# Optimization experiments

Measured on AMD Instinct MI355X. Metric: run time of the kernel, lower is better.

The kernel has to match this reference:

```python
import jax, jax.numpy as jnp
import numpy as np

N, E, D_IN, HID, HEADS, TS_OUT = 100000, 200000, 165, 64, 8, 5
HD1 = HID // HEADS  # 8 per-head channels in layer 1
HD2 = HID           # 64 per-head channels in layer 2 (concat=False -> mean)


def _glorot(key, shape):
    fan_in, fan_out = shape[0], shape[1]
    s = np.sqrt(6.0 / (fan_in + fan_out)).astype(np.float32)
    return jax.random.uniform(key, shape, jnp.float32, -s, s)


def setup_inputs() -> dict:
    key = jax.random.key(0)
    ks = jax.random.split(key, 24)
    inp = {
        "x": jax.random.normal(ks[0], (N, D_IN), jnp.float32),
        "edge_index": jax.random.randint(ks[1], (2, E), 0, N, jnp.int32),
        "timestamp_target": jax.random.randint(ks[2], (N,), 0, TS_OUT, jnp.int32),
        "node_target": jax.random.randint(ks[3], (N,), 0, 2, jnp.int32),
        "node_mask": jax.random.randint(ks[4], (N,), 0, 2, jnp.int32).astype(jnp.bool_),
        # GATConv layer 1: in=165 -> 8 heads x 8 ch, concat -> 64
        "W1": _glorot(ks[5], (D_IN, HEADS * HD1)),
        "att_src1": _glorot(ks[6], (HEADS, HD1)),
        "att_dst1": _glorot(ks[7], (HEADS, HD1)),
        "b1": jnp.zeros((HEADS * HD1,), jnp.float32),
        # GATConv layer 2: in=64 -> 8 heads x 64 ch, mean -> 64
        "W2": _glorot(ks[8], (HID, HEADS * HD2)),
        "att_src2": _glorot(ks[9], (HEADS, HD2)),
        "att_dst2": _glorot(ks[10], (HEADS, HD2)),
        "b2": jnp.zeros((HD2,), jnp.float32),
        # timestamp predictor MLP
        "ts_w1": _glorot(ks[11], (HID, HID)), "ts_b1": jnp.zeros((HID,), jnp.float32),
        "ts_w2": _glorot(ks[12], (HID, TS_OUT)), "ts_b2": jnp.zeros((TS_OUT,), jnp.float32),
        # class predictor MLP
        "cls_w1": _glorot(ks[13], (HID, HID)), "cls_b1": jnp.zeros((HID,), jnp.float32),
        "cls_w2": _glorot(ks[14], (HID, 2)), "cls_b2": jnp.zeros((2,), jnp.float32),
    }
    return inp


def _gat_layer(x, src, dst, n, W, a_src, a_dst, b, concat):
    H, C = a_src.shape
    h = (x @ W).reshape(n, H, C)                      # [N,H,C]
    a_s = (h * a_src).sum(-1)                         # [N,H]
    a_d = (h * a_dst).sum(-1)                         # [N,H]
    alpha = jax.nn.leaky_relu(a_s[src] + a_d[dst], 0.2)   # [E,H]
    amax = jax.ops.segment_max(alpha, dst, num_segments=n)
    ea = jnp.exp(alpha - amax[dst])
    denom = jax.ops.segment_sum(ea, dst, num_segments=n)
    a = ea / (denom[dst] + 1e-16)                     # segment softmax over incoming edges
    out = jax.ops.segment_sum(h[src] * a[:, :, None], dst, num_segments=n)  # [N,H,C]
    out = out.reshape(n, H * C) if concat else out.mean(axis=1)
    return out + b


def _ce(logits, targets):
    lp = jax.nn.log_softmax(logits, axis=-1)
    return -jnp.take_along_axis(lp, targets[:, None].astype(jnp.int32), axis=1)[:, 0]


def reference(x, edge_index, timestamp_target, node_target, node_mask,
              W1, att_src1, att_dst1, b1, W2, att_src2, att_dst2, b2,
              ts_w1, ts_b1, ts_w2, ts_b2, cls_w1, cls_b1, cls_w2, cls_b2):
    n = x.shape[0]
    loops = jnp.arange(n, dtype=edge_index.dtype)
    src = jnp.concatenate([edge_index[0], loops])     # add self loops (PyG default)
    dst = jnp.concatenate([edge_index[1], loops])
    h = _gat_layer(x, src, dst, n, W1, att_src1, att_dst1, b1, True)   # [N,64]
    h = _gat_layer(h, src, dst, n, W2, att_src2, att_dst2, b2, False)  # [N,64]
    # gradient reversal is identity in the forward pass
    ts_pred = jax.nn.relu(h @ ts_w1 + ts_b1) @ ts_w2 + ts_b2           # [N,5]
    cls_pred = jax.nn.relu(h @ cls_w1 + cls_b1) @ cls_w2 + cls_b2      # [N,2]
    ts_loss = _ce(ts_pred, timestamp_target).mean()
    m = node_mask.astype(jnp.float32)
    cls_loss = (_ce(cls_pred, node_target) * m).sum() / m.sum()
    return cls_loss + 1.0 * ts_loss
```

## Files before the change

### kernel.cpp

```cpp
#include <hip/hip_runtime.h>
#include <hip/hip_bf16.h>

#define NN 100000
#define NE 200000
#define NT (NE + NN)
#define DIN 165
#define PREPB 128
#define INITB 391
#define PACKB 32
#define W1PB 24
#define MISCGRID (PREPB + INITB + PACKB + W1PB)
#define NODEB 1563
#define XDW ((size_t)NN * DIN)
#define G1ROWS 32
#define G1NDMA 21
#define L2ROWS 32

typedef __attribute__((ext_vector_type(8))) short bf16x8_t;
typedef __attribute__((ext_vector_type(4))) float f32x4_t;
typedef _Float16 h2_t __attribute__((ext_vector_type(2)));
typedef _Float16 f16x8_t __attribute__((ext_vector_type(8)));

#define AS1 __attribute__((address_space(1)))
#define AS3 __attribute__((address_space(3)))

static __device__ __forceinline__ unsigned short f2bf(float f) {
    __hip_bfloat16 b = __float2bfloat16(f);
    return *(unsigned short*)&b;
}
static __device__ __forceinline__ float bfu(unsigned short u) {
    __hip_bfloat16 b = *(__hip_bfloat16*)&u;
    return __bfloat162float(b);
}
static __device__ __forceinline__ unsigned pkh2(float a, float b) {
    h2_t v; v[0] = (_Float16)a; v[1] = (_Float16)b;
    return *(unsigned*)&v;
}


__global__ __launch_bounds__(256) void k_misc(const float* W2, const float* a2s, const float* a2d,
                                              float* wsd, __hip_bfloat16* W2pT,
                                              int* cnt, int* fill,
                                              const float* tsw1, const float* cw1,
                                              __hip_bfloat16* wB,
                                              const float* W1, unsigned* W1pT, float* zbuf) {
    int b = blockIdx.x;
    int tid = threadIdx.x;
    if (b < PREPB) {
        int i = b * 256 + tid;
        int c = i >> 9, j = i & 511;
        int hh = j >> 6, kk = j & 63;
        W2pT[i] = __float2bfloat16(W2[kk * 512 + hh * 64 + c]);
        if (b == 0) zbuf[tid] = 0.f;
        if (i < 512) {
            int h = i >> 6, k = i & 63;
            float s = 0.f, d = 0.f;
            for (int cc = 0; cc < 64; cc++) {
                float w = W2[k * 512 + h * 64 + cc];
                s += w * a2s[h * 64 + cc];
                d += w * a2d[h * 64 + cc];
            }
            wsd[i] = s; wsd[512 + i] = d;
        }
    } else if (b < PREPB + INITB) {
        int i = (b - PREPB) * 256 + tid;
        if (i < NN) { cnt[i] = 0; fill[i] = 0; }
    } else if (b < PREPB + INITB + PACKB) {
        int i = (b - PREPB - INITB) * 256 + tid;
        if (i < 8192) {
            int c = i >> 6, k = i & 63;
            float v = (c < 64) ? tsw1[k * 64 + c] : cw1[k * 64 + (c - 64)];
            wB[i] = __float2bfloat16(v);
        }
    } else {
        int i = (b - PREPB - INITB - PACKB) * 256 + tid;
        if (i < 6144) {
            int c = i / 96, kp = i - c * 96;
            int k = 2 * kp;
            float f0 = (k < DIN) ? W1[k * 64 + c] : 0.f;
            float f1 = (k + 1 < DIN) ? W1[(k + 1) * 64 + c] : 0.f;
            W1pT[i] = pkh2(f0, f1);
        }
    }
}


__global__ __launch_bounds__(256) void k_count(const int* dstE, int* cnt) {
    int e = blockIdx.x * 256 + threadIdx.x;
    if (e < NE) atomicAdd(&cnt[dstE[e]], 1);
}

__global__ __launch_bounds__(256) void k_scanA(const int* cnt, int* rowptr, int* bsum) {
    __shared__ int sm[256];
    int t = threadIdx.x;
    int base = blockIdx.x * 1024;
    int v[4]; int s = 0;
    for (int i = 0; i < 4; i++) {
        int idx = base + t * 4 + i;
        v[i] = (idx < NN) ? (cnt[idx] + 1) : 0;
        s += v[i];
    }
    sm[t] = s; __syncthreads();
    for (int off = 1; off < 256; off <<= 1) {
        int x = (t >= off) ? sm[t - off] : 0;
        __syncthreads();
        sm[t] += x;
        __syncthreads();
    }
    int run = sm[t] - s;
    for (int i = 0; i < 4; i++) {
        run += v[i];
        int idx = base + t * 4 + i;
        if (idx < NN) rowptr[idx + 1] = run;
    }
    if (t == 255) bsum[blockIdx.x] = sm[255];
}

__global__ __launch_bounds__(64) void k_scanB(int* bsum, int nb) {
    int lane = threadIdx.x;
    int v0 = (lane < nb) ? bsum[lane] : 0;
    int v1 = (64 + lane < nb) ? bsum[64 + lane] : 0;
    int s0 = v0;
    for (int off = 1; off < 64; off <<= 1) { int t = __shfl_up(s0, off); if (lane >= off) s0 += t; }
    int tot0 = __shfl(s0, 63);
    int s1 = v1;
    for (int off = 1; off < 64; off <<= 1) { int t = __shfl_up(s1, off); if (lane >= off) s1 += t; }
    if (lane < nb) bsum[lane] = s0 - v0;
    if (64 + lane < nb) bsum[64 + lane] = tot0 + s1 - v1;
}

__global__ __launch_bounds__(256) void k_scanC(const int* bsum, int* rowptr) {
    int i = blockIdx.x * 256 + threadIdx.x;
    if (i < NN) rowptr[i + 1] += bsum[i >> 10];
    if (i == 0) rowptr[0] = 0;
}

__global__ __launch_bounds__(256) void k_fill(const int* srcE, const int* dstE,
                                              const int* rowptr, int* fill, int* col, int* rowv) {
    int i = blockIdx.x * 256 + threadIdx.x;
    if (i >= NT) return;
    int s, d;
    if (i < NE) { s = srcE[i]; d = dstE[i]; }
    else        { s = i - NE; d = s; }
    int p = rowptr[d] + atomicAdd(&fill[d], 1);
    col[p] = s;
    rowv[p] = d;
}


__global__ __launch_bounds__(128) void k_gemm1(const float* x, const unsigned* W1pT,
                                               const float* att_s, const float* att_d,
                                               const float* zsrc,
                                               __hip_bfloat16* h1b, float* aad1) {
    __shared__ float X[G1NDMA * 256];
    int tid = threadIdx.x;
    int l = tid & 63, w = tid >> 6;
    int n0 = blockIdx.x * G1ROWS;
    int frow = l & 15, kg = l >> 4;

    size_t tb = (size_t)n0 * DIN;
    for (int i = w; i < G1NDMA; i += 2) {
        size_t gd = tb + (size_t)i * 256 + (size_t)l * 4;
        const float* g = (gd + 4 <= XDW) ? (x + gd) : (zsrc + l * 4);
        __builtin_amdgcn_global_load_lds((const AS1 float*)g,
                                         (AS3 float*)(X + i * 256), 16, 0, 0);
    }
    uint4 B[6][4];
    #pragma unroll
    for (int s = 0; s < 6; s++)
        #pragma unroll
        for (int t = 0; t < 4; t++)
            B[s][t] = *(const uint4*)&W1pT[(t * 16 + frow) * 96 + s * 16 + kg * 4];
    __syncthreads();

    f32x4_t acc[4] = {};
    int rbase = (w * 16 + frow) * DIN + kg * 8;
    #pragma unroll
    for (int s = 0; s < 6; s++) {
        f16x8_t av;
        #pragma unroll
        for (int j = 0; j < 8; j++) av[j] = (_Float16)X[rbase + s * 32 + j];
        #pragma unroll
        for (int t = 0; t < 4; t++)
            acc[t] = __builtin_amdgcn_mfma_f32_16x16x32_f16(av, *(f16x8_t*)&B[s][t], acc[t], 0, 0, 0);
    }

    int nw = n0 + w * 16;
    float asv[4], adv[4];
    #pragma unroll
    for (int t = 0; t < 4; t++) {
        int c = t * 16 + frow;
        asv[t] = att_s[c]; adv[t] = att_d[c];
    }
    int hb = (l >> 3) & 1;
    #pragma unroll
    for (int q = 0; q < 4; q++) {
        int n = nw + kg * 4 + q;
        #pragma unroll
        for (int t = 0; t < 4; t++) {
            float sv = acc[t][q] * asv[t];
            float dv = acc[t][q] * adv[t];
            sv += __shfl_xor(sv, 1); sv += __shfl_xor(sv, 2); sv += __shfl_xor(sv, 4);
            dv += __shfl_xor(dv, 1); dv += __shfl_xor(dv, 2); dv += __shfl_xor(dv, 4);
            if ((l & 7) == 0) {
                int h = t * 2 + hb;
                aad1[(size_t)n * 16 + h]     = sv;
                aad1[(size_t)n * 16 + 8 + h] = dv;
            }
        }
    }

    __syncthreads();
    unsigned short* Hw = (unsigned short*)X + w * 1152;
    #pragma unroll
    for (int t = 0; t < 4; t++)
        #pragma unroll
        for (int q = 0; q < 4; q++)
            Hw[(kg * 4 + q) * 72 + t * 16 + frow] = f2bf(acc[t][q]);
    int rr = l >> 2, cc = l & 3;
    int n2 = nw + rr;
    unsigned short* dst = (unsigned short*)h1b + (size_t)n2 * 64 + cc * 16;
    *(uint4*)dst       = *(const uint4*)&Hw[rr * 72 + cc * 16];
    *(uint4*)(dst + 8) = *(const uint4*)&Hw[rr * 72 + cc * 16 + 8];
}


__global__ __launch_bounds__(256) void k_edgew(const float* aad, const int* col, const int* rowv,
                                               __hip_bfloat16* web) {
    int e = blockIdx.x * 256 + threadIdx.x;
    if (e >= NT) return;
    int s = col[e], d = rowv[e];
    float4 s0 = *(const float4*)&aad[(size_t)s * 16];
    float4 s1 = *(const float4*)&aad[(size_t)s * 16 + 4];
    float4 dd0 = *(const float4*)&aad[(size_t)d * 16 + 8];
    float4 dd1 = *(const float4*)&aad[(size_t)d * 16 + 12];
    float as[8] = {s0.x, s0.y, s0.z, s0.w, s1.x, s1.y, s1.z, s1.w};
    float ad[8] = {dd0.x, dd0.y, dd0.z, dd0.w, dd1.x, dd1.y, dd1.z, dd1.w};
    unsigned p[4];
    #pragma unroll
    for (int q = 0; q < 4; q++) {
        float a0 = as[2*q]   + ad[2*q];
        float a1 = as[2*q+1] + ad[2*q+1];
        a0 = a0 > 0.f ? a0 : 0.2f * a0;
        a1 = a1 > 0.f ? a1 : 0.2f * a1;
        p[q] = (unsigned)f2bf(__expf(a0)) | ((unsigned)f2bf(__expf(a1)) << 16);
    }
    *(uint4*)&web[(size_t)e * 8] = make_uint4(p[0], p[1], p[2], p[3]);
}


__global__ __launch_bounds__(256) void k_agg1(const __hip_bfloat16* h1b, const __hip_bfloat16* we1b,
                                              const int* rowptr, const int* col,
                                              const float* b1, __hip_bfloat16* out1b) {
    int tid = threadIdx.x;
    int q = tid & 15;
    int n = blockIdx.x * 16 + (tid >> 4);
    int hq = q >> 1;
    const unsigned short* h1u = (const unsigned short*)h1b;
    const unsigned short* weu = (const unsigned short*)we1b;
    int rs = rowptr[n], re = rowptr[n + 1];
    float acc0 = 0.f, acc1 = 0.f, acc2 = 0.f, acc3 = 0.f, den = 0.f;
    for (int eb = rs; eb < re; eb += 4) {
        int c4[4];
        #pragma unroll
        for (int j = 0; j < 4; j++) c4[j] = col[min(eb + j, re - 1)];
        #pragma unroll
        for (int j = 0; j < 4; j++) {
            int e = min(eb + j, re - 1);
            float wv = bfu(weu[(size_t)e * 8 + hq]);
            wv = (eb + j < re) ? wv : 0.f;
            uint2 hv = *(const uint2*)&h1u[(size_t)c4[j] * 64 + q * 4];
            den  += wv;
            acc0 += wv * bfu((unsigned short)(hv.x & 0xffff));
            acc1 += wv * bfu((unsigned short)(hv.x >> 16));
            acc2 += wv * bfu((unsigned short)(hv.y & 0xffff));
            acc3 += wv * bfu((unsigned short)(hv.y >> 16));
        }
    }
    float4 bb = *(const float4*)&b1[q * 4];
    float dd = den + 1e-16f;
    unsigned short* ou = (unsigned short*)out1b;
    unsigned p0 = (unsigned)f2bf(acc0 / dd + bb.x) | ((unsigned)f2bf(acc1 / dd + bb.y) << 16);
    unsigned p1 = (unsigned)f2bf(acc2 / dd + bb.z) | ((unsigned)f2bf(acc3 / dd + bb.w) << 16);
    *(uint2*)&ou[(size_t)n * 64 + q * 4] = make_uint2(p0, p1);
}


__global__ __launch_bounds__(256) void k_att2(const __hip_bfloat16* out1b, const float* wsd,
                                              float* aad2) {
    __shared__ float t[64][65];
    int tid = threadIdx.x;
    int n0 = blockIdx.x * 64;
    const unsigned short* o1u = (const unsigned short*)out1b;
    #pragma unroll
    for (int l = 0; l < 4; l++) {
        int q = tid + l * 256;
        int r = q >> 4, c4 = q & 15;
        int n = n0 + r;
        uint2 v = make_uint2(0, 0);
        if (n < NN) v = *(const uint2*)&o1u[(size_t)n * 64 + c4 * 4];
        t[r][c4 * 4 + 0] = bfu((unsigned short)(v.x & 0xffff));
        t[r][c4 * 4 + 1] = bfu((unsigned short)(v.x >> 16));
        t[r][c4 * 4 + 2] = bfu((unsigned short)(v.y & 0xffff));
        t[r][c4 * 4 + 3] = bfu((unsigned short)(v.y >> 16));
    }
    __syncthreads();
    int lane = tid & 63;
    int j0 = __builtin_amdgcn_readfirstlane((tid >> 6) * 4);
    int n = n0 + lane;
    float a0 = 0.f, a1 = 0.f, a2 = 0.f, a3 = 0.f;
    #pragma unroll 8
    for (int k = 0; k < 64; k++) {
        float ov = t[lane][k];
        a0 += ov * wsd[(j0 + 0) * 64 + k];
        a1 += ov * wsd[(j0 + 1) * 64 + k];
        a2 += ov * wsd[(j0 + 2) * 64 + k];
        a3 += ov * wsd[(j0 + 3) * 64 + k];
    }
    if (n < NN) *(float4*)&aad2[(size_t)n * 16 + j0] = make_float4(a0, a1, a2, a3);
}


__global__ __launch_bounds__(256) void k_l2f(const __hip_bfloat16* out1b, const __hip_bfloat16* we2b,
                                             const int* rowptr, const int* col,
                                             const __hip_bfloat16* W2pT, const float* b2,
                                             const __hip_bfloat16* wB,
                                             const float* tsb1, const float* cb1,
                                             const float* tsw2, const float* tsb2,
                                             const float* cw2, const float* cb2,
                                             const int* tst, const int* ctg, const unsigned char* msk,
                                             float* part) {
    __shared__ unsigned short Ax[L2ROWS * 512];
    __shared__ float red[4][3];
    int tid = threadIdx.x;
    int l = tid & 63, w = tid >> 6;
    int n0 = blockIdx.x * L2ROWS;
    int frow = l & 15, kg = l >> 4;

    const unsigned short* o1u = (const unsigned short*)out1b;
    const unsigned short* weu = (const unsigned short*)we2b;
    int q4 = tid & 15;
    #pragma unroll 1
    for (int pass = 0; pass < 2; pass++) {
        int j = pass * 16 + (tid >> 4);
        int n = n0 + j;
        int rs = rowptr[n], re = rowptr[n + 1];
        float acc[8][4];
        float den[8];
        #pragma unroll
        for (int h = 0; h < 8; h++) {
            den[h] = 0.f;
            #pragma unroll
            for (int c = 0; c < 4; c++) acc[h][c] = 0.f;
        }
        for (int eb = rs; eb < re; eb += 4) {
            int c4[4];
            #pragma unroll
            for (int jj = 0; jj < 4; jj++) c4[jj] = col[min(eb + jj, re - 1)];
            #pragma unroll
            for (int jj = 0; jj < 4; jj++) {
                int e = min(eb + jj, re - 1);
                uint4 wv = *(const uint4*)&weu[(size_t)e * 8];
                uint2 hv = *(const uint2*)&o1u[(size_t)c4[jj] * 64 + q4 * 4];
                float vm = (eb + jj < re) ? 1.f : 0.f;
                float hc0 = bfu((unsigned short)(hv.x & 0xffff));
                float hc1 = bfu((unsigned short)(hv.x >> 16));
                float hc2 = bfu((unsigned short)(hv.y & 0xffff));
                float hc3 = bfu((unsigned short)(hv.y >> 16));
                float wt[8] = {bfu((unsigned short)(wv.x & 0xffff)), bfu((unsigned short)(wv.x >> 16)),
                               bfu((unsigned short)(wv.y & 0xffff)), bfu((unsigned short)(wv.y >> 16)),
                               bfu((unsigned short)(wv.z & 0xffff)), bfu((unsigned short)(wv.z >> 16)),
                               bfu((unsigned short)(wv.w & 0xffff)), bfu((unsigned short)(wv.w >> 16))};
                #pragma unroll
                for (int h = 0; h < 8; h++) {
                    float ww = wt[h] * vm;
                    den[h] += ww;
                    acc[h][0] += ww * hc0;
                    acc[h][1] += ww * hc1;
                    acc[h][2] += ww * hc2;
                    acc[h][3] += ww * hc3;
                }
            }
        }
        #pragma unroll
        for (int h = 0; h < 8; h++) {
            float dd = den[h] + 1e-16f;
            unsigned lo = (unsigned)f2bf(acc[h][0] / dd) | ((unsigned)f2bf(acc[h][1] / dd) << 16);
            unsigned hi = (unsigned)f2bf(acc[h][2] / dd) | ((unsigned)f2bf(acc[h][3] / dd) << 16);
            int blk = (h * 8 + (q4 >> 1)) ^ (j & 7);
            *(uint2*)&Ax[j * 512 + blk * 8 + (q4 & 1) * 4] = make_uint2(lo, hi);
        }
    }
    __syncthreads();

    const unsigned short* Bg = (const unsigned short*)W2pT;
    int r0 = (w & 1) * 16;
    int c0 = (w >> 1) * 32;
    f32x4_t gacc[2] = {};
    uint4 rBa00, rBa01, rBa10, rBa11;
    rBa00 = *(const uint4*)&Bg[(size_t)(c0 + frow) * 512 + 0 * 32 + kg * 8];
    rBa01 = *(const uint4*)&Bg[(size_t)(c0 + frow) * 512 + 1 * 32 + kg * 8];
    rBa10 = *(const uint4*)&Bg[(size_t)(c0 + 16 + frow) * 512 + 0 * 32 + kg * 8];
    rBa11 = *(const uint4*)&Bg[(size_t)(c0 + 16 + frow) * 512 + 1 * 32 + kg * 8];
    #pragma unroll
    for (int k0 = 0; k0 < 512; k0 += 64) {
        uint4 rBb00, rBb01, rBb10, rBb11;
        if (k0 < 448) {
            int kn = k0 + 64;
            rBb00 = *(const uint4*)&Bg[(size_t)(c0 + frow) * 512 + kn + 0 * 32 + kg * 8];
            rBb01 = *(const uint4*)&Bg[(size_t)(c0 + frow) * 512 + kn + 1 * 32 + kg * 8];
            rBb10 = *(const uint4*)&Bg[(size_t)(c0 + 16 + frow) * 512 + kn + 0 * 32 + kg * 8];
            rBb11 = *(const uint4*)&Bg[(size_t)(c0 + 16 + frow) * 512 + kn + 1 * 32 + kg * 8];
        }
        #pragma unroll
        for (int kk = 0; kk < 2; kk++) {
            int bidx = (k0 >> 3) + kk * 4 + kg;
            int blk = bidx ^ (frow & 7);
            bf16x8_t a = *(const bf16x8_t*)&Ax[(r0 + frow) * 512 + blk * 8];
            gacc[0] = __builtin_amdgcn_mfma_f32_16x16x32_bf16(
                a, *(bf16x8_t*)(kk == 0 ? &rBa00 : &rBa01), gacc[0], 0, 0, 0);
            gacc[1] = __builtin_amdgcn_mfma_f32_16x16x32_bf16(
                a, *(bf16x8_t*)(kk == 0 ? &rBa10 : &rBa11), gacc[1], 0, 0, 0);
        }
        rBa00 = rBb00; rBa01 = rBb01; rBa10 = rBb10; rBa11 = rBb11;
    }
    __syncthreads();

    unsigned short* o2L = Ax;
    #pragma unroll
    for (int t = 0; t < 2; t++) {
        float bias = b2[c0 + t * 16 + frow];
        f32x4_t g = gacc[t];
        #pragma unroll
        for (int q = 0; q < 4; q++)
            o2L[(r0 + kg * 4 + q) * 72 + c0 + t * 16 + frow] = f2bf(0.125f * g[q] + bias);
    }
    __syncthreads();
    const unsigned short* wBu = (const unsigned short*)wB;
    int m0 = (w & 1) * 16;
    int h0 = (w >> 1) * 64;
    f32x4_t a2c[4] = {};
    #pragma unroll
    for (int kk = 0; kk < 2; kk++) {
        bf16x8_t a2 = *(const bf16x8_t*)&o2L[(m0 + frow) * 72 + kk * 32 + kg * 8];
        #pragma unroll
        for (int t2 = 0; t2 < 4; t2++) {
            bf16x8_t bf = *(const bf16x8_t*)&wBu[(h0 + t2 * 16 + frow) * 64 + kk * 32 + kg * 8];
            a2c[t2] = __builtin_amdgcn_mfma_f32_16x16x32_bf16(a2, bf, a2c[t2], 0, 0, 0);
        }
    }

    float tsl = 0.f, cll = 0.f, mval = 0.f;
    if ((w >> 1) == 0) {
        float lg[4][5];
        #pragma unroll
        for (int q = 0; q < 4; q++)
            #pragma unroll
            for (int t = 0; t < 5; t++) lg[q][t] = 0.f;
        #pragma unroll
        for (int t2 = 0; t2 < 4; t2++) {
            int c = t2 * 16 + frow;
            float bb = tsb1[c];
            float w0 = tsw2[c * 5 + 0], w1 = tsw2[c * 5 + 1], w2 = tsw2[c * 5 + 2],
                  w3 = tsw2[c * 5 + 3], w4 = tsw2[c * 5 + 4];
            #pragma unroll
            for (int q = 0; q < 4; q++) {
                float v = fmaxf(a2c[t2][q] + bb, 0.f);
                lg[q][0] += v * w0; lg[q][1] += v * w1; lg[q][2] += v * w2;
                lg[q][3] += v * w3; lg[q][4] += v * w4;
            }
        }
        #pragma unroll
        for (int q = 0; q < 4; q++)
            #pragma unroll
            for (int t = 0; t < 5; t++) {
                lg[q][t] += __shfl_xor(lg[q][t], 1);
                lg[q][t] += __shfl_xor(lg[q][t], 2);
                lg[q][t] += __shfl_xor(lg[q][t], 4);
                lg[q][t] += __shfl_xor(lg[q][t], 8);
            }
        if (frow == 0) {
            #pragma unroll
            for (int q = 0; q < 4; q++) {
                int n = n0 + m0 + kg * 4 + q;
                float L[5];
                #pragma unroll
                for (int t = 0; t < 5; t++) L[t] = lg[q][t] + tsb2[t];
                float mx = fmaxf(fmaxf(fmaxf(L[0], L[1]), fmaxf(L[2], L[3])), L[4]);
                float se = 0.f;
                #pragma unroll
                for (int t = 0; t < 5; t++) se += __expf(L[t] - mx);
                int tg = tst[n];
                float pick = 0.f;
                #pragma unroll
                for (int t = 0; t < 5; t++) pick += (t == tg) ? L[t] : 0.f;
                tsl += mx + __logf(se) - pick;
            }
        }
    } else {
        float lc[4][2];
        #pragma unroll
        for (int q = 0; q < 4; q++) { lc[q][0] = 0.f; lc[q][1] = 0.f; }
        #pragma unroll
        for (int t2 = 0; t2 < 4; t2++) {
            int c = t2 * 16 + frow;
            float bb = cb1[c];
            float u0 = cw2[c * 2], u1 = cw2[c * 2 + 1];
            #pragma unroll
            for (int q = 0; q < 4; q++) {
                float v = fmaxf(a2c[t2][q] + bb, 0.f);
                lc[q][0] += v * u0; lc[q][1] += v * u1;
            }
        }
        #pragma unroll
        for (int q = 0; q < 4; q++)
            #pragma unroll
            for (int t = 0; t < 2; t++) {
                lc[q][t] += __shfl_xor(lc[q][t], 1);
                lc[q][t] += __shfl_xor(lc[q][t], 2);
                lc[q][t] += __shfl_xor(lc[q][t], 4);
                lc[q][t] += __shfl_xor(lc[q][t], 8);
            }
        if (frow == 0) {
            #pragma unroll
            for (int q = 0; q < 4; q++) {
                int n = n0 + m0 + kg * 4 + q;
                float C0 = lc[q][0] + cb2[0];
                float C1 = lc[q][1] + cb2[1];
                float mx2 = fmaxf(C0, C1);
                float lse2 = mx2 + __logf(__expf(C0 - mx2) + __expf(C1 - mx2));
                float mv = msk[n] ? 1.f : 0.f;
                float pick2 = ctg[n] ? C1 : C0;
                cll += (lse2 - pick2) * mv;
                mval += mv;
            }
        }
    }
    #pragma unroll
    for (int off = 1; off < 64; off <<= 1) {
        tsl  += __shfl_xor(tsl, off);
        cll  += __shfl_xor(cll, off);
        mval += __shfl_xor(mval, off);
    }
    if (l == 0) { red[w][0] = tsl; red[w][1] = cll; red[w][2] = mval; }
    __syncthreads();
    if (tid == 0) {
        part[blockIdx.x * 3 + 0] = red[0][0] + red[1][0] + red[2][0] + red[3][0];
        part[blockIdx.x * 3 + 1] = red[0][1] + red[1][1] + red[2][1] + red[3][1];
        part[blockIdx.x * 3 + 2] = red[0][2] + red[1][2] + red[2][2] + red[3][2];
    }
}

__global__ __launch_bounds__(256) void k_final(const float* part, float* out, int nb) {
    __shared__ float sm[3][256];
    int tid = threadIdx.x;
    float a = 0, b = 0, c = 0;
    for (int i = tid; i < nb; i += 256) { a += part[i*3]; b += part[i*3+1]; c += part[i*3+2]; }
    sm[0][tid] = a; sm[1][tid] = b; sm[2][tid] = c;
    __syncthreads();
    for (int s = 128; s > 0; s >>= 1) {
        if (tid < s) {
            sm[0][tid] += sm[0][tid + s];
            sm[1][tid] += sm[1][tid + s];
            sm[2][tid] += sm[2][tid + s];
        }
        __syncthreads();
    }
    if (tid == 0) out[0] = sm[1][0] / sm[2][0] + sm[0][0] / (float)NN;
}


extern "C" void kernel_launch(void* const* d_in, const int* in_sizes, int n_in,
                              void* d_out, int out_size, void* d_ws, size_t ws_size,
                              hipStream_t stream) {
    const float* x    = (const float*)d_in[0];
    const int*   ei   = (const int*)d_in[1];
    const int*   tst  = (const int*)d_in[2];
    const int*   ctg  = (const int*)d_in[3];
    const unsigned char* msk = (const unsigned char*)d_in[4];
    const float* W1   = (const float*)d_in[5];
    const float* a1s  = (const float*)d_in[6];
    const float* a1d  = (const float*)d_in[7];
    const float* b1   = (const float*)d_in[8];
    const float* W2   = (const float*)d_in[9];
    const float* a2s  = (const float*)d_in[10];
    const float* a2d  = (const float*)d_in[11];
    const float* b2   = (const float*)d_in[12];
    const float* tsw1 = (const float*)d_in[13];
    const float* tsb1 = (const float*)d_in[14];
    const float* tsw2 = (const float*)d_in[15];
    const float* tsb2 = (const float*)d_in[16];
    const float* cw1  = (const float*)d_in[17];
    const float* cb1  = (const float*)d_in[18];
    const float* cw2  = (const float*)d_in[19];
    const float* cb2  = (const float*)d_in[20];
    const int* srcE = ei;
    const int* dstE = ei + NE;

    char* ws = (char*)d_ws;
    size_t off = 0;
    auto alloc = [&](size_t b) { size_t o = off; off = (off + b + 255) & ~(size_t)255; return o; };
    int*   cnt    = (int*)(ws + alloc((size_t)NN * 4));
    int*   fill   = (int*)(ws + alloc((size_t)NN * 4));
    int*   rowptr = (int*)(ws + alloc((size_t)(NN + 1) * 4));
    int*   bsum   = (int*)(ws + alloc(128 * 4));
    int*   col    = (int*)(ws + alloc((size_t)NT * 4));
    int*   rowv   = (int*)(ws + alloc((size_t)NT * 4));
    float* aad1   = (float*)(ws + alloc((size_t)NN * 16 * 4));
    __hip_bfloat16* out1b = (__hip_bfloat16*)(ws + alloc((size_t)NN * 64 * 2));
    float* aad2   = (float*)(ws + alloc((size_t)NN * 16 * 4));
    float* wsd    = (float*)(ws + alloc(1024 * 4));
    __hip_bfloat16* W2pT  = (__hip_bfloat16*)(ws + alloc(32768 * 2));
    __hip_bfloat16* wB    = (__hip_bfloat16*)(ws + alloc(8192 * 2));
    unsigned* W1pT = (unsigned*)(ws + alloc(6144 * 4));
    float* zbuf   = (float*)(ws + alloc(256 * 4));
    __hip_bfloat16* h1b   = (__hip_bfloat16*)(ws + alloc((size_t)NN * 64 * 2));
    __hip_bfloat16* web   = (__hip_bfloat16*)(ws + alloc((size_t)NT * 8 * 2));
    float* part   = (float*)(ws + alloc((size_t)(NN / L2ROWS) * 3 * 4));
    (void)ws_size; (void)in_sizes; (void)n_in; (void)out_size;

    int nb_scan = (NN + 1023) / 1024;

    k_misc<<<MISCGRID, 256, 0, stream>>>(W2, a2s, a2d, wsd, W2pT, cnt, fill,
                                         tsw1, cw1, wB, W1, W1pT, zbuf);
    k_count<<<(NE + 255) / 256, 256, 0, stream>>>(dstE, cnt);
    k_scanA<<<nb_scan, 256, 0, stream>>>(cnt, rowptr, bsum);
    k_scanB<<<1, 64, 0, stream>>>(bsum, nb_scan);
    k_scanC<<<(NN + 255) / 256, 256, 0, stream>>>(bsum, rowptr);
    k_fill<<<(NT + 255) / 256, 256, 0, stream>>>(srcE, dstE, rowptr, fill, col, rowv);

    k_gemm1<<<NN / G1ROWS, 128, 0, stream>>>(x, W1pT, a1s, a1d, zbuf, h1b, aad1);
    k_edgew<<<(NT + 255) / 256, 256, 0, stream>>>(aad1, col, rowv, web);
    k_agg1<<<NN / 16, 256, 0, stream>>>(h1b, web, rowptr, col, b1, out1b);
    k_att2<<<NODEB, 256, 0, stream>>>(out1b, wsd, aad2);
    k_edgew<<<(NT + 255) / 256, 256, 0, stream>>>(aad2, col, rowv, web);

    k_l2f<<<NN / L2ROWS, 256, 0, stream>>>(out1b, web, rowptr, col, W2pT, b2, wB,
                                           tsb1, cb1, tsw2, tsb2, cw2, cb2, tst, ctg, msk, part);

    k_final<<<1, 256, 0, stream>>>(part, (float*)d_out, NN / L2ROWS);
}
```

Measured before the change: 199.7 us.

## Fuse att2 into agg1 and split layer-2 aggregation from GEMM in chunks

Computes the layer-2 attention projections inside the layer-1 aggregation kernel with a 16-lane shuffle reduction, which removes the separate att2 kernel and one reread of out1b. The fused layer-2 kernel is split in two. A gather-aggregate kernel writes swizzled bf16 rows to a workspace buffer, and a GEMM+MLP+loss kernel loads those rows into LDS with global_load_lds. This is done in two node chunks to bound the buffer size. The split lets each phase run at its own occupancy, at the cost of extra global traffic (about 50 MB written and read per chunk) and more kernel launches.

```diff
diff --git a/kernel.cpp b/kernel.cpp
--- a/kernel.cpp
+++ b/kernel.cpp
@@ -10,11 +10,11 @@
 #define PACKB 32
 #define W1PB 24
 #define MISCGRID (PREPB + INITB + PACKB + W1PB)
-#define NODEB 1563
 #define XDW ((size_t)NN * DIN)
 #define G1ROWS 32
 #define G1NDMA 21
-#define L2ROWS 32
+#define CHUNKA 49984
+#define GPARTS 3125
 
 typedef __attribute__((ext_vector_type(8))) short bf16x8_t;
 typedef __attribute__((ext_vector_type(4))) float f32x4_t;
@@ -249,9 +249,10 @@
 }
 
 
-__global__ __launch_bounds__(256) void k_agg1(const __hip_bfloat16* h1b, const __hip_bfloat16* we1b,
-                                              const int* rowptr, const int* col,
-                                              const float* b1, __hip_bfloat16* out1b) {
+__global__ __launch_bounds__(256) void k_agg1f(const __hip_bfloat16* h1b, const __hip_bfloat16* we1b,
+                                               const int* rowptr, const int* col,
+                                               const float* b1, const float* wsd,
+                                               __hip_bfloat16* out1b, float* aad2) {
     int tid = threadIdx.x;
     int q = tid & 15;
     int n = blockIdx.x * 16 + (tid >> 4);
@@ -279,117 +280,107 @@
     }
     float4 bb = *(const float4*)&b1[q * 4];
     float dd = den + 1e-16f;
+    unsigned short u0 = f2bf(acc0 / dd + bb.x);
+    unsigned short u1 = f2bf(acc1 / dd + bb.y);
+    unsigned short u2 = f2bf(acc2 / dd + bb.z);
+    unsigned short u3 = f2bf(acc3 / dd + bb.w);
     unsigned short* ou = (unsigned short*)out1b;
-    unsigned p0 = (unsigned)f2bf(acc0 / dd + bb.x) | ((unsigned)f2bf(acc1 / dd + bb.y) << 16);
-    unsigned p1 = (unsigned)f2bf(acc2 / dd + bb.z) | ((unsigned)f2bf(acc3 / dd + bb.w) << 16);
-    *(uint2*)&ou[(size_t)n * 64 + q * 4] = make_uint2(p0, p1);
-}
-
-
-__global__ __launch_bounds__(256) void k_att2(const __hip_bfloat16* out1b, const float* wsd,
-                                              float* aad2) {
-    __shared__ float t[64][65];
+    *(uint2*)&ou[(size_t)n * 64 + q * 4] =
+        make_uint2((unsigned)u0 | ((unsigned)u1 << 16), (unsigned)u2 | ((unsigned)u3 << 16));
+
+    float r0 = bfu(u0), r1 = bfu(u1), r2 = bfu(u2), r3 = bfu(u3);
+    float p[16];
+    #pragma unroll
+    for (int j = 0; j < 16; j++) {
+        float4 wv = *(const float4*)&wsd[j * 64 + q * 4];
+        p[j] = r0 * wv.x + r1 * wv.y + r2 * wv.z + r3 * wv.w;
+    }
+    #pragma unroll
+    for (int s = 1; s < 16; s <<= 1)
+        #pragma unroll
+        for (int j = 0; j < 16; j++) p[j] += __shfl_xor(p[j], s);
+    float myp = 0.f;
+    #pragma unroll
+    for (int j = 0; j < 16; j++) myp = (q == j) ? p[j] : myp;
+    aad2[(size_t)n * 16 + q] = myp;
+}
+
+
+__global__ __launch_bounds__(256) void k_agg2f(const __hip_bfloat16* out1b, const __hip_bfloat16* we2b,
+                                               const int* rowptr, const int* col,
+                                               __hip_bfloat16* aggb, int n0c) {
     int tid = threadIdx.x;
-    int n0 = blockIdx.x * 64;
+    int q4 = tid & 15;
+    int nl = blockIdx.x * 16 + (tid >> 4);
+    int n = n0c + nl;
     const unsigned short* o1u = (const unsigned short*)out1b;
-    #pragma unroll
-    for (int l = 0; l < 4; l++) {
-        int q = tid + l * 256;
-        int r = q >> 4, c4 = q & 15;
-        int n = n0 + r;
-        uint2 v = make_uint2(0, 0);
-        if (n < NN) v = *(const uint2*)&o1u[(size_t)n * 64 + c4 * 4];
-        t[r][c4 * 4 + 0] = bfu((unsigned short)(v.x & 0xffff));
-        t[r][c4 * 4 + 1] = bfu((unsigned short)(v.x >> 16));
-        t[r][c4 * 4 + 2] = bfu((unsigned short)(v.y & 0xffff));
-        t[r][c4 * 4 + 3] = bfu((unsigned short)(v.y >> 16));
-    }
-    __syncthreads();
-    int lane = tid & 63;
-    int j0 = __builtin_amdgcn_readfirstlane((tid >> 6) * 4);
-    int n = n0 + lane;
-    float a0 = 0.f, a1 = 0.f, a2 = 0.f, a3 = 0.f;
-    #pragma unroll 8
-    for (int k = 0; k < 64; k++) {
-        float ov = t[lane][k];
-        a0 += ov * wsd[(j0 + 0) * 64 + k];
-        a1 += ov * wsd[(j0 + 1) * 64 + k];
-        a2 += ov * wsd[(j0 + 2) * 64 + k];
-        a3 += ov * wsd[(j0 + 3) * 64 + k];
-    }
-    if (n < NN) *(float4*)&aad2[(size_t)n * 16 + j0] = make_float4(a0, a1, a2, a3);
-}
-
-
-__global__ __launch_bounds__(256) void k_l2f(const __hip_bfloat16* out1b, const __hip_bfloat16* we2b,
-                                             const int* rowptr, const int* col,
+    const unsigned short* weu = (const unsigned short*)we2b;
+    int rs = rowptr[n], re = rowptr[n + 1];
+    float den[8] = {};
+    float acc[8][4] = {};
+    for (int eb = rs; eb < re; eb += 4) {
+        int c4[4];
+        #pragma unroll
+        for (int jj = 0; jj < 4; jj++) c4[jj] = col[min(eb + jj, re - 1)];
+        #pragma unroll
+        for (int jj = 0; jj < 4; jj++) {
+            int e = min(eb + jj, re - 1);
+            uint4 wv = *(const uint4*)&weu[(size_t)e * 8];
+            uint2 hv = *(const uint2*)&o1u[(size_t)c4[jj] * 64 + q4 * 4];
+            float vm = (eb + jj < re) ? 1.f : 0.f;
+            float hc0 = bfu((unsigned short)(hv.x & 0xffff));
+            float hc1 = bfu((unsigned short)(hv.x >> 16));
+            float hc2 = bfu((unsigned short)(hv.y & 0xffff));
+            float hc3 = bfu((unsigned short)(hv.y >> 16));
+            float wt[8] = {bfu((unsigned short)(wv.x & 0xffff)), bfu((unsigned short)(wv.x >> 16)),
+                           bfu((unsigned short)(wv.y & 0xffff)), bfu((unsigned short)(wv.y >> 16)),
+                           bfu((unsigned short)(wv.z & 0xffff)), bfu((unsigned short)(wv.z >> 16)),
+                           bfu((unsigned short)(wv.w & 0xffff)), bfu((unsigned short)(wv.w >> 16))};
+            #pragma unroll
+            for (int h = 0; h < 8; h++) {
+                float ww = wt[h] * vm;
+                den[h] += ww;
+                acc[h][0] += ww * hc0;
+                acc[h][1] += ww * hc1;
+                acc[h][2] += ww * hc2;
+                acc[h][3] += ww * hc3;
+            }
+        }
+    }
+    unsigned short* au = (unsigned short*)aggb;
+    size_t base = (size_t)nl * 512;
+    #pragma unroll
+    for (int h = 0; h < 8; h++) {
+        float ddv = den[h] + 1e-16f;
+        unsigned lo = (unsigned)f2bf(acc[h][0] / ddv) | ((unsigned)f2bf(acc[h][1] / ddv) << 16);
+        unsigned hi = (unsigned)f2bf(acc[h][2] / ddv) | ((unsigned)f2bf(acc[h][3] / ddv) << 16);
+        int blk = (h * 8 + (q4 >> 1)) ^ (nl & 7);
+        *(uint2*)&au[base + blk * 8 + (q4 & 1) * 4] = make_uint2(lo, hi);
+    }
+}
+
+
+__global__ __launch_bounds__(256) void k_g2m(const __hip_bfloat16* aggb,
                                              const __hip_bfloat16* W2pT, const float* b2,
                                              const __hip_bfloat16* wB,
                                              const float* tsb1, const float* cb1,
                                              const float* tsw2, const float* tsb2,
                                              const float* cw2, const float* cb2,
                                              const int* tst, const int* ctg, const unsigned char* msk,
-                                             float* part) {
-    __shared__ unsigned short Ax[L2ROWS * 512];
+                                             float* part, int n0c, int pbase) {
+    __shared__ unsigned short Ax[32 * 512];
     __shared__ float red[4][3];
     int tid = threadIdx.x;
     int l = tid & 63, w = tid >> 6;
-    int n0 = blockIdx.x * L2ROWS;
+    int nl0 = blockIdx.x * 32;
+    int n0 = n0c + nl0;
     int frow = l & 15, kg = l >> 4;
 
-    const unsigned short* o1u = (const unsigned short*)out1b;
-    const unsigned short* weu = (const unsigned short*)we2b;
-    int q4 = tid & 15;
-    #pragma unroll 1
-    for (int pass = 0; pass < 2; pass++) {
-        int j = pass * 16 + (tid >> 4);
-        int n = n0 + j;
-        int rs = rowptr[n], re = rowptr[n + 1];
-        float acc[8][4];
-        float den[8];
-        #pragma unroll
-        for (int h = 0; h < 8; h++) {
-            den[h] = 0.f;
-            #pragma unroll
-            for (int c = 0; c < 4; c++) acc[h][c] = 0.f;
-        }
-        for (int eb = rs; eb < re; eb += 4) {
-            int c4[4];
-            #pragma unroll
-            for (int jj = 0; jj < 4; jj++) c4[jj] = col[min(eb + jj, re - 1)];
-            #pragma unroll
-            for (int jj = 0; jj < 4; jj++) {
-                int e = min(eb + jj, re - 1);
-                uint4 wv = *(const uint4*)&weu[(size_t)e * 8];
-                uint2 hv = *(const uint2*)&o1u[(size_t)c4[jj] * 64 + q4 * 4];
-                float vm = (eb + jj < re) ? 1.f : 0.f;
-                float hc0 = bfu((unsigned short)(hv.x & 0xffff));
-                float hc1 = bfu((unsigned short)(hv.x >> 16));
-                float hc2 = bfu((unsigned short)(hv.y & 0xffff));
-                float hc3 = bfu((unsigned short)(hv.y >> 16));
-                float wt[8] = {bfu((unsigned short)(wv.x & 0xffff)), bfu((unsigned short)(wv.x >> 16)),
-                               bfu((unsigned short)(wv.y & 0xffff)), bfu((unsigned short)(wv.y >> 16)),
-                               bfu((unsigned short)(wv.z & 0xffff)), bfu((unsigned short)(wv.z >> 16)),
-                               bfu((unsigned short)(wv.w & 0xffff)), bfu((unsigned short)(wv.w >> 16))};
-                #pragma unroll
-                for (int h = 0; h < 8; h++) {
-                    float ww = wt[h] * vm;
-                    den[h] += ww;
-                    acc[h][0] += ww * hc0;
-                    acc[h][1] += ww * hc1;
-                    acc[h][2] += ww * hc2;
-                    acc[h][3] += ww * hc3;
-                }
-            }
-        }
-        #pragma unroll
-        for (int h = 0; h < 8; h++) {
-            float dd = den[h] + 1e-16f;
-            unsigned lo = (unsigned)f2bf(acc[h][0] / dd) | ((unsigned)f2bf(acc[h][1] / dd) << 16);
-            unsigned hi = (unsigned)f2bf(acc[h][2] / dd) | ((unsigned)f2bf(acc[h][3] / dd) << 16);
-            int blk = (h * 8 + (q4 >> 1)) ^ (j & 7);
-            *(uint2*)&Ax[j * 512 + blk * 8 + (q4 & 1) * 4] = make_uint2(lo, hi);
-        }
+    const unsigned short* ag = (const unsigned short*)aggb;
+    for (int i = w; i < 32; i += 4) {
+        const float* src = (const float*)(ag + (size_t)(nl0 + i) * 512) + l * 4;
+        __builtin_amdgcn_global_load_lds((const AS1 float*)src,
+                                         (AS3 float*)((float*)Ax + i * 256), 16, 0, 0);
     }
     __syncthreads();
 
@@ -545,9 +536,10 @@
     if (l == 0) { red[w][0] = tsl; red[w][1] = cll; red[w][2] = mval; }
     __syncthreads();
     if (tid == 0) {
-        part[blockIdx.x * 3 + 0] = red[0][0] + red[1][0] + red[2][0] + red[3][0];
-        part[blockIdx.x * 3 + 1] = red[0][1] + red[1][1] + red[2][1] + red[3][1];
-        part[blockIdx.x * 3 + 2] = red[0][2] + red[1][2] + red[2][2] + red[3][2];
+        int pb = pbase + blockIdx.x;
+        part[pb * 3 + 0] = red[0][0] + red[1][0] + red[2][0] + red[3][0];
+        part[pb * 3 + 1] = red[0][1] + red[1][1] + red[2][1] + red[3][1];
+        part[pb * 3 + 2] = red[0][2] + red[1][2] + red[2][2] + red[3][2];
     }
 }
 
@@ -616,7 +608,8 @@
     float* zbuf   = (float*)(ws + alloc(256 * 4));
     __hip_bfloat16* h1b   = (__hip_bfloat16*)(ws + alloc((size_t)NN * 64 * 2));
     __hip_bfloat16* web   = (__hip_bfloat16*)(ws + alloc((size_t)NT * 8 * 2));
-    float* part   = (float*)(ws + alloc((size_t)(NN / L2ROWS) * 3 * 4));
+    __hip_bfloat16* aggb  = (__hip_bfloat16*)(ws + alloc((size_t)(NN - CHUNKA) * 512 * 2));
+    float* part   = (float*)(ws + alloc((size_t)GPARTS * 3 * 4));
     (void)ws_size; (void)in_sizes; (void)n_in; (void)out_size;
 
     int nb_scan = (NN + 1023) / 1024;
@@ -631,12 +624,21 @@
 
     k_gemm1<<<NN / G1ROWS, 128, 0, stream>>>(x, W1pT, a1s, a1d, zbuf, h1b, aad1);
     k_edgew<<<(NT + 255) / 256, 256, 0, stream>>>(aad1, col, rowv, web);
-    k_agg1<<<NN / 16, 256, 0, stream>>>(h1b, web, rowptr, col, b1, out1b);
-    k_att2<<<NODEB, 256, 0, stream>>>(out1b, wsd, aad2);
+    k_agg1f<<<NN / 16, 256, 0, stream>>>(h1b, web, rowptr, col, b1, wsd, out1b, aad2);
     k_edgew<<<(NT + 255) / 256, 256, 0, stream>>>(aad2, col, rowv, web);
 
-    k_l2f<<<NN / L2ROWS, 256, 0, stream>>>(out1b, web, rowptr, col, W2pT, b2, wB,
-                                           tsb1, cb1, tsw2, tsb2, cw2, cb2, tst, ctg, msk, part);
-
-    k_final<<<1, 256, 0, stream>>>(part, (float*)d_out, NN / L2ROWS);
-}
+    {
+        int n0c = 0, sz = CHUNKA, pbase = 0;
+        k_agg2f<<<sz / 16, 256, 0, stream>>>(out1b, web, rowptr, col, aggb, n0c);
+        k_g2m<<<sz / 32, 256, 0, stream>>>(aggb, W2pT, b2, wB, tsb1, cb1, tsw2, tsb2,
+                                           cw2, cb2, tst, ctg, msk, part, n0c, pbase);
+    }
+    {
+        int n0c = CHUNKA, sz = NN - CHUNKA, pbase = CHUNKA / 32;
+        k_agg2f<<<sz / 16, 256, 0, stream>>>(out1b, web, rowptr, col, aggb, n0c);
+        k_g2m<<<sz / 32, 256, 0, stream>>>(aggb, W2pT, b2, wB, tsb1, cb1, tsw2, tsb2,
+                                           cw2, cb2, tst, ctg, msk, part, n0c, pbase);
+    }
+
+    k_final<<<1, 256, 0, stream>>>(part, (float*)d_out, GPARTS);
+}
```

After: 249.0 us. 24.7% more time.
